# Performance work log

Hardware: AMD Instinct MI355X
Metric: run time of the kernel (lower is better)

The kernel has to match this reference:

```python
import jax, jax.numpy as jnp
import numpy as np

K = 3
STRIDE = 1
PAD = 1
DIL = 1


def _conv2d(x, w, b, stride, pad):
    y = jax.lax.conv_general_dilated(
        x, w, (stride, stride), [(pad, pad), (pad, pad)],
        dimension_numbers=('NCHW', 'OIHW', 'NCHW'))
    return y + b[None, :, None, None]


def setup_inputs() -> dict:
    key = jax.random.key(0)
    ks = jax.random.split(key, 6)
    N, Cin, Cout, H, W = 4, 64, 64, 128, 128
    x = jax.random.normal(ks[0], (N, Cin, H, W), jnp.float32)
    w_off = jax.random.normal(ks[1], (2 * K * K, Cin, K, K), jnp.float32) * 0.01
    b_off = jnp.zeros((2 * K * K,), jnp.float32)
    w_mask = jax.random.normal(ks[2], (K * K, Cin, K, K), jnp.float32) * 0.01
    b_mask = jnp.zeros((K * K,), jnp.float32)
    weight = jax.random.normal(ks[3], (Cout, Cin, K, K), jnp.float32) * 0.05
    bias = jax.random.normal(ks[4], (Cout,), jnp.float32)
    return {"x": x, "w_off": w_off, "b_off": b_off,
            "w_mask": w_mask, "b_mask": b_mask,
            "weight": weight, "bias": bias}


def _deform_conv(x, offset, weight, bias):
    # x: [N,C,H,W]; offset: [N,2*K2,Ho,Wo] with channel layout (dy,dx) per kernel pt
    N, C, H, W = x.shape
    K2 = K * K
    Ho, Wo = offset.shape[2], offset.shape[3]
    off_y = offset[:, 0::2]  # [N,K2,Ho,Wo]
    off_x = offset[:, 1::2]
    ki = jnp.arange(K2) // K
    kj = jnp.arange(K2) % K
    base_y = (jnp.arange(Ho) * STRIDE - PAD)[None, :, None] + (ki * DIL)[:, None, None]
    base_x = (jnp.arange(Wo) * STRIDE - PAD)[None, None, :] + (kj * DIL)[:, None, None]
    py = base_y[None].astype(off_y.dtype) + off_y  # [N,K2,Ho,Wo]
    px = base_x[None].astype(off_x.dtype) + off_x
    y0 = jnp.floor(py)
    x0 = jnp.floor(px)
    wy = py - y0
    wx = px - x0
    xf = x.reshape(N, C, H * W)

    def corner(yi, xi):
        valid = (yi >= 0) & (yi <= H - 1) & (xi >= 0) & (xi <= W - 1)
        yc = jnp.clip(yi, 0, H - 1).astype(jnp.int32)
        xc = jnp.clip(xi, 0, W - 1).astype(jnp.int32)
        idx = (yc * W + xc).reshape(N, -1)  # [N, K2*Ho*Wo]
        g = jnp.take_along_axis(xf, idx[:, None, :], axis=2)  # [N,C,K2*Ho*Wo]
        g = g.reshape(N, C, K2, Ho, Wo)
        return g * valid[:, None].astype(x.dtype)

    # bilinear interpolation with zero padding outside the image
    val = ((1 - wy) * (1 - wx))[:, None] * corner(y0, x0) \
        + ((1 - wy) * wx)[:, None] * corner(y0, x0 + 1) \
        + (wy * (1 - wx))[:, None] * corner(y0 + 1, x0) \
        + (wy * wx)[:, None] * corner(y0 + 1, x0 + 1)  # [N,C,K2,Ho,Wo]
    out = jnp.einsum('nckhw,ock->nohw', val,
                     weight.reshape(weight.shape[0], C, K2))
    return out + bias[None, :, None, None]


def reference(x, w_off, b_off, w_mask, b_mask, weight, bias):
    offset = _conv2d(x, w_off, b_off, STRIDE, PAD)              # [N,2*K2,Ho,Wo]
    mask = jax.nn.sigmoid(_conv2d(x, w_mask, b_mask, STRIDE, PAD))  # [N,K2,Ho,Wo]
    # source does mask.repeat(1,2,1,1) then offset*mask, then plain deform_conv2d
    offset = offset * jnp.concatenate([mask, mask], axis=1)
    return _deform_conv(x, offset, weight, bias)
```

## Files before the change

### kernel.cpp

```cpp
#include <hip/hip_runtime.h>
#include <math.h>

#define HD 128
#define WD 128
#define WP 130
#define CIN 64
#define COUT 64
#define NB 4
#define K2 9
#define HW (HD*WD)
#define CK 576
#define TP 16
#define NKK 18

#define WAM   (4 * NKK * 64 * 8)
#define WAO   (2 * NKK * 64 * 8)
#define XTP   ((size_t)NB * WP * WP * CIN)
#define OFFSZ ((size_t)NB * K2 * HW)
#define WTSZ  ((size_t)CK * COUT)

#define PRE_T 1024
#define PRE_H 65
#define PRE_P ((WAM + WAO) / 256)
#define HALO_PER_N 33024
#define HALO_W8 16512

typedef __attribute__((ext_vector_type(8))) short short8;
typedef __attribute__((ext_vector_type(4))) float f32x4;

__device__ inline unsigned short f2bf(float v) {
    unsigned int u = __float_as_uint(v);
    unsigned int r = u + 0x7fffu + ((u >> 16) & 1u);
    return (unsigned short)(r >> 16);
}
__device__ inline float bf2f(unsigned short b) {
    return __uint_as_float(((unsigned int)b) << 16);
}
__device__ inline unsigned int pack_bf16(float a, float b) {
#if __has_builtin(__builtin_amdgcn_cvt_pk_bf16_f32)
    auto r = __builtin_amdgcn_cvt_pk_bf16_f32(a, b);
    unsigned int u; __builtin_memcpy(&u, &r, 4); return u;
#else
    return ((unsigned int)f2bf(b) << 16) | (unsigned int)f2bf(a);
#endif
}

__global__ __launch_bounds__(256) void pre_kernel(
    const float* __restrict__ x,
    const float* __restrict__ weight,
    const float* __restrict__ w_off,
    const float* __restrict__ w_mask,
    unsigned short* __restrict__ xp,
    short* __restrict__ mhi, short* __restrict__ mlo,
    short* __restrict__ ohi, short* __restrict__ olo)
{
    __shared__ float tile[64][66];
    int bid = blockIdx.x;
    int t = threadIdx.x;

    if (bid < PRE_T) {
        int half = bid & 1;
        int h = (bid >> 1) & 127;
        int n = bid >> 8;
        int w0 = half * 64;
        int g = t >> 6, wl = t & 63;
        const float* xb = x + ((size_t)n * CIN) * HW + h * WD + w0;
        #pragma unroll
        for (int i = 0; i < 16; i++) {
            int cc = i * 4 + g;
            tile[wl][cc] = xb[(size_t)cc * HW + wl];
        }
        __syncthreads();
        size_t rowbase = (((size_t)n * WP + (h + 1)) * WP + (w0 + 1)) * CIN;
        #pragma unroll
        for (int i = 0; i < 8; i++) {
            int u = i * 256 + t;
            int ww = u >> 5;
            int cp = (u & 31) * 2;
            float2 v = *(const float2*)&tile[ww][cp];
            *(unsigned int*)&xp[rowbase + (size_t)ww * CIN + cp] = pack_bf16(v.x, v.y);
        }
    } else if (bid < PRE_T + PRE_H) {
        int widx = (bid - PRE_T) * 256 + t;
        if (widx < HALO_W8) {
            int s = widx * 8;
            int n = s / HALO_PER_N;
            int v = s - n * HALO_PER_N;
            size_t nb = (size_t)n * WP * WP * CIN;
            size_t base;
            if (v < 8320) {
                base = nb + v;
            } else if (v < 16640) {
                base = nb + (size_t)129 * WP * CIN + (v - 8320);
            } else if (v < 24832) {
                int v2 = v - 16640; int h = 1 + (v2 >> 6); int c = v2 & 63;
                base = nb + (size_t)h * WP * CIN + c;
            } else {
                int v3 = v - 24832; int h = 1 + (v3 >> 6); int c = v3 & 63;
                base = nb + ((size_t)h * WP + 129) * CIN + c;
            }
            short8 z = {0, 0, 0, 0, 0, 0, 0, 0};
            *(short8*)&xp[base] = z;
        }
    } else {
        int gid = (bid - PRE_T - PRE_H) * 256 + t;
        if (gid < WAM) {
            int idx = gid;
            int jj = idx & 7;
            int lane = (idx >> 3) & 63;
            int kk = (idx >> 9) % NKK;
            int mt = (idx >> 9) / NKK;
            int o = mt * 16 + (lane & 15);
            int rp = kk * 32 + (lane >> 4) * 8 + jj;
            int k = rp >> 6, c = rp & 63;
            float w = weight[((size_t)o * CIN + c) * 9 + k];
            unsigned short h = f2bf(w);
            mhi[idx] = (short)h;
            mlo[idx] = (short)f2bf(w - bf2f(h));
        } else {
            int idx = gid - WAM;
            int jj = idx & 7;
            int lane = (idx >> 3) & 63;
            int kk = (idx >> 9) % NKK;
            int mt = (idx >> 9) / NKK;
            int j = mt * 16 + (lane & 15);
            int rp = kk * 32 + (lane >> 4) * 8 + jj;
            int k = rp >> 6, c = rp & 63;
            float w = 0.f;
            if (j < 18)      w = w_off[((size_t)j * CIN + c) * 9 + k];
            else if (j < 27) w = w_mask[((size_t)(j - 18) * CIN + c) * 9 + k];
            unsigned short h = f2bf(w);
            ohi[idx] = (short)h;
            olo[idx] = (short)f2bf(w - bf2f(h));
        }
    }
}

__global__ __launch_bounds__(256) void fused_kernel(
    const unsigned short* __restrict__ xp,
    const short* __restrict__ waM_hi, const short* __restrict__ waM_lo,
    const short* __restrict__ waO_hi, const short* __restrict__ waO_lo,
    const float* __restrict__ b_off, const float* __restrict__ b_mask,
    const float* __restrict__ bias,
    float* __restrict__ out)
{
    __shared__ __align__(16) short val_hi[72 * 128];
    __shared__ float conv_s[27 * 17];
    __shared__ float4 p_w4[K2 * TP];
    __shared__ int4   p_idx4[K2 * TP];

    int t = threadIdx.x;
    int wv = t >> 6;
    int lane = t & 63;
    int wo0 = blockIdx.x * TP;
    int ho  = blockIdx.y;
    int n   = blockIdx.z;
    const unsigned short* xpn = xp + (size_t)n * WP * WP * CIN;
    int p16 = lane & 15, quad = lane >> 4;

    #pragma unroll
    for (int i = 0; i < 5; i++) {
        int u = t + 256 * i;
        if (u < K2 * TP * 8) {
            int tap = u >> 7;
            int p = (u >> 3) & 15;
            int g = u & 7;
            int ti = tap / 3, tj = tap - ti * 3;
            const short8 v = *(const short8*)&xpn[((size_t)(ho + ti) * WP + (wo0 + p + tj)) * CIN + g * 8];
            int c2 = tap * 8 + g;
            *(short8*)&val_hi[c2 * 128 + ((p + c2) & 15) * 8] = v;
        }
    }
    __syncthreads();

    if (wv < 2) {
        f32x4 acc = {0.f, 0.f, 0.f, 0.f};
        for (int kk = 0; kk < NKK; kk++) {
            int abase = ((wv * NKK + kk) * 64 + lane) * 8;
            short8 ah = *(const short8*)&waO_hi[abase];
            short8 al = *(const short8*)&waO_lo[abase];
            int c2 = kk * 4 + quad;
            short8 b = *(const short8*)&val_hi[c2 * 128 + ((p16 + c2) & 15) * 8];
            acc = __builtin_amdgcn_mfma_f32_16x16x32_bf16(ah, b, acc, 0, 0, 0);
            acc = __builtin_amdgcn_mfma_f32_16x16x32_bf16(al, b, acc, 0, 0, 0);
        }
        #pragma unroll
        for (int i = 0; i < 4; i++) {
            int j = wv * 16 + quad * 4 + i;
            if (j < 27) {
                float bv = (j < 18) ? b_off[j] : b_mask[j - 18];
                conv_s[j * 17 + p16] = acc[i] + bv;
            }
        }
    }
    __syncthreads();

    if (t < K2 * TP) {
        int k = t >> 4, p = t & 15;
        float oy_raw = conv_s[(2 * k) * 17 + p];
        float ox_raw = conv_s[(2 * k + 1) * 17 + p];
        float my = 1.f / (1.f + expf(-conv_s[(18 + (2 * k) % 9) * 17 + p]));
        float mx = 1.f / (1.f + expf(-conv_s[(18 + (2 * k + 1) % 9) * 17 + p]));
        float oy = oy_raw * my;
        float ox = ox_raw * mx;
        int ki = k / 3, kj = k - ki * 3;
        int wo = wo0 + p;
        float py = (float)(ho - 1 + ki) + oy;
        float px = (float)(wo - 1 + kj) + ox;
        float y0f = floorf(py), x0f = floorf(px);
        float wy = py - y0f, wx = px - x0f;
        int y0 = (int)y0f, x0 = (int)x0f;
        float wy0 = 1.f - wy, wx0 = 1.f - wx;
        int y0c = min(max(y0, 0), HD - 1);
        int y1c = min(max(y0 + 1, 0), HD - 1);
        int x0c = min(max(x0, 0), WD - 1);
        int x1c = min(max(x0 + 1, 0), WD - 1);
        bool vy0 = (y0 >= 0) && (y0 < HD);
        bool vy1 = (y0 + 1 >= 0) && (y0 + 1 < HD);
        bool vx0 = (x0 >= 0) && (x0 < WD);
        bool vx1 = (x0 + 1 >= 0) && (x0 + 1 < WD);
        float4 w4;
        w4.x = (vy0 && vx0) ? wy0 * wx0 : 0.f;
        w4.y = (vy0 && vx1) ? wy0 * wx  : 0.f;
        w4.z = (vy1 && vx0) ? wy  * wx0 : 0.f;
        w4.w = (vy1 && vx1) ? wy  * wx  : 0.f;
        int4 i4;
        i4.x = ((y0c + 1) * WP + (x0c + 1)) * CIN;
        i4.y = ((y0c + 1) * WP + (x1c + 1)) * CIN;
        i4.z = ((y1c + 1) * WP + (x0c + 1)) * CIN;
        i4.w = ((y1c + 1) * WP + (x1c + 1)) * CIN;
        p_w4[t] = w4;
        p_idx4[t] = i4;
    }
    __syncthreads();

    {
        int sub = lane >> 4;
        int c0 = (lane & 15) * 4;
        #pragma unroll
        for (int i = 0; i < 9; i++) {
            int task = i * 16 + wv * 4 + sub;
            int k = task >> 4, p = task & 15;
            float4 w4 = p_w4[task];
            int4  i4 = p_idx4[task];
            uint2 qa = *(const uint2*)&xpn[i4.x + c0];
            uint2 qb = *(const uint2*)&xpn[i4.y + c0];
            uint2 qc = *(const uint2*)&xpn[i4.z + c0];
            uint2 qd = *(const uint2*)&xpn[i4.w + c0];
            float g0 = w4.x * __uint_as_float(qa.x << 16)
                     + w4.y * __uint_as_float(qb.x << 16)
                     + w4.z * __uint_as_float(qc.x << 16)
                     + w4.w * __uint_as_float(qd.x << 16);
            float g1 = w4.x * __uint_as_float(qa.x & 0xffff0000u)
                     + w4.y * __uint_as_float(qb.x & 0xffff0000u)
                     + w4.z * __uint_as_float(qc.x & 0xffff0000u)
                     + w4.w * __uint_as_float(qd.x & 0xffff0000u);
            float g2 = w4.x * __uint_as_float(qa.y << 16)
                     + w4.y * __uint_as_float(qb.y << 16)
                     + w4.z * __uint_as_float(qc.y << 16)
                     + w4.w * __uint_as_float(qd.y << 16);
            float g3 = w4.x * __uint_as_float(qa.y & 0xffff0000u)
                     + w4.y * __uint_as_float(qb.y & 0xffff0000u)
                     + w4.z * __uint_as_float(qc.y & 0xffff0000u)
                     + w4.w * __uint_as_float(qd.y & 0xffff0000u);
            uint2 r;
            r.x = pack_bf16(g0, g1);
            r.y = pack_bf16(g2, g3);
            int c2 = k * 8 + (c0 >> 3);
            int jj = c0 & 7;
            *(uint2*)&val_hi[c2 * 128 + ((p + c2) & 15) * 8 + jj] = r;
        }
    }
    __syncthreads();

    f32x4 acc = {0.f, 0.f, 0.f, 0.f};
    for (int kk = 0; kk < NKK; kk++) {
        int abase = ((wv * NKK + kk) * 64 + lane) * 8;
        short8 ah = *(const short8*)&waM_hi[abase];
        short8 al = *(const short8*)&waM_lo[abase];
        int c2 = kk * 4 + quad;
        short8 b = *(const short8*)&val_hi[c2 * 128 + ((p16 + c2) & 15) * 8];
        acc = __builtin_amdgcn_mfma_f32_16x16x32_bf16(ah, b, acc, 0, 0, 0);
        acc = __builtin_amdgcn_mfma_f32_16x16x32_bf16(al, b, acc, 0, 0, 0);
    }
    __syncthreads();
    float* os = (float*)val_hi;
    #pragma unroll
    for (int i = 0; i < 4; i++) {
        int o = wv * 16 + quad * 4 + i;
        os[o * 17 + p16] = acc[i] + bias[o];
    }
    __syncthreads();

    size_t obase = ((size_t)n * COUT) * HW + (size_t)ho * WD + wo0;
    #pragma unroll
    for (int i = 0; i < 4; i++) {
        int l = t + 256 * i;
        int oo = l >> 4, p = l & 15;
        out[obase + (size_t)oo * HW + p] = os[oo * 17 + p];
    }
}

__global__ void transpose_w_kernel(const float* __restrict__ w, float* __restrict__ wt) {
    int i = blockIdx.x * 256 + threadIdx.x;
    int o = i / CK;
    int ck = i - o * CK;
    wt[ck * COUT + o] = w[i];
}

__global__ __launch_bounds__(256) void offmask_kernel(
    const float* __restrict__ x,
    const float* __restrict__ w_off, const float* __restrict__ b_off,
    const float* __restrict__ w_mask, const float* __restrict__ b_mask,
    float* __restrict__ offy, float* __restrict__ offx)
{
    __shared__ float ws[CK][27];
    int t = threadIdx.x;
    for (int i = t; i < CK * 27; i += 256) {
        int j = i % 27;
        int citap = i / 27;
        int ci = citap / 9;
        int tap = citap - ci * 9;
        float v;
        if (j < 18) v = w_off[(j * CIN + ci) * 9 + tap];
        else        v = w_mask[((j - 18) * CIN + ci) * 9 + tap];
        ws[citap][j] = v;
    }
    __syncthreads();

    int pix = blockIdx.x * 256 + t;
    int n  = pix >> 14;
    int ho = (pix >> 7) & 127;
    int wo = pix & 127;

    float acc[27];
    #pragma unroll
    for (int j = 0; j < 18; j++) acc[j] = b_off[j];
    #pragma unroll
    for (int j = 0; j < 9; j++)  acc[18 + j] = b_mask[j];

    int offs[9];
    bool oks[9];
    #pragma unroll
    for (int dy = 0; dy < 3; dy++) {
        int y = ho - 1 + dy;
        #pragma unroll
        for (int dx = 0; dx < 3; dx++) {
            int xx = wo - 1 + dx;
            bool ok = (y >= 0) && (y < HD) && (xx >= 0) && (xx < WD);
            oks[dy * 3 + dx] = ok;
            offs[dy * 3 + dx] = (ok ? y : 0) * WD + (ok ? xx : 0);
        }
    }
    const float* xn = x + (size_t)n * CIN * HW;
    for (int ci = 0; ci < CIN; ci++) {
        const float* xc = xn + (size_t)ci * HW;
        float v[9];
        #pragma unroll
        for (int tap = 0; tap < 9; tap++)
            v[tap] = oks[tap] ? xc[offs[tap]] : 0.f;
        #pragma unroll
        for (int tap = 0; tap < 9; tap++) {
            const float* wrow = ws[ci * 9 + tap];
            float vv = v[tap];
            #pragma unroll
            for (int j = 0; j < 27; j++) acc[j] += wrow[j] * vv;
        }
    }
    float m[9];
    #pragma unroll
    for (int j = 0; j < 9; j++) m[j] = 1.f / (1.f + expf(-acc[18 + j]));
    #pragma unroll
    for (int k = 0; k < 9; k++) {
        int cy = 2 * k, cx = 2 * k + 1;
        float my = m[cy < 9 ? cy : cy - 9];
        float mx = m[cx < 9 ? cx : cx - 9];
        size_t o = (((size_t)n * K2 + k) * HD + ho) * WD + wo;
        offy[o] = acc[cy] * my;
        offx[o] = acc[cx] * mx;
    }
}

__global__ __launch_bounds__(256) void deform_kernel(
    const float* __restrict__ x,
    const float* __restrict__ offy, const float* __restrict__ offx,
    const float* __restrict__ wt,
    const float* __restrict__ bias,
    float* __restrict__ out)
{
    __shared__ __align__(16) float val_s[CK * TP];
    __shared__ float4 p_w4[K2 * TP];
    __shared__ int4   p_idx4[K2 * TP];

    int t = threadIdx.x;
    int wo0 = blockIdx.x * TP;
    int ho  = blockIdx.y;
    int n   = blockIdx.z;

    if (t < K2 * TP) {
        int k = t >> 4, p = t & 15;
        int wo = wo0 + p;
        size_t oi = (((size_t)n * K2 + k) * HD + ho) * WD + wo;
        float oy = offy[oi], ox = offx[oi];
        int ki = k / 3, kj = k - ki * 3;
        float py = (float)(ho - 1 + ki) + oy;
        float px = (float)(wo - 1 + kj) + ox;
        float y0f = floorf(py), x0f = floorf(px);
        float wy = py - y0f, wx = px - x0f;
        int y0 = (int)y0f, x0 = (int)x0f;
        float wy0 = 1.f - wy, wx0 = 1.f - wx;
        int y0c = min(max(y0, 0), HD - 1);
        int y1c = min(max(y0 + 1, 0), HD - 1);
        int x0c = min(max(x0, 0), WD - 1);
        int x1c = min(max(x0 + 1, 0), WD - 1);
        bool vy0 = (y0 >= 0) && (y0 < HD);
        bool vy1 = (y0 + 1 >= 0) && (y0 + 1 < HD);
        bool vx0 = (x0 >= 0) && (x0 < WD);
        bool vx1 = (x0 + 1 >= 0) && (x0 + 1 < WD);
        float4 w4;
        w4.x = (vy0 && vx0) ? wy0 * wx0 : 0.f;
        w4.y = (vy0 && vx1) ? wy0 * wx  : 0.f;
        w4.z = (vy1 && vx0) ? wy  * wx0 : 0.f;
        w4.w = (vy1 && vx1) ? wy  * wx  : 0.f;
        int4 i4;
        i4.x = y0c * WD + x0c;
        i4.y = y0c * WD + x1c;
        i4.z = y1c * WD + x0c;
        i4.w = y1c * WD + x1c;
        p_w4[t] = w4;
        p_idx4[t] = i4;
    }
    __syncthreads();

    const float* xn = x + (size_t)n * CIN * HW;
    for (int e = t; e < CK * TP; e += 256) {
        int row = e >> 4, p = e & 15;
        int cc = row / 9, k = row - cc * 9;
        int task = (k << 4) | p;
        float4 w4 = p_w4[task];
        int4  i4 = p_idx4[task];
        const float* xc = xn + (size_t)cc * HW;
        val_s[e] = w4.x * xc[i4.x] + w4.y * xc[i4.y]
                 + w4.z * xc[i4.z] + w4.w * xc[i4.w];
    }
    __syncthreads();

    int o = t & 63, q = t >> 6;
    float4 acc = {0.f, 0.f, 0.f, 0.f};
    const float4* v4 = (const float4*)val_s;
    const float* wp = wt + o;
    #pragma unroll 4
    for (int r = 0; r < CK; r++) {
        float w = wp[r * COUT];
        float4 vv = v4[r * 4 + q];
        acc.x += w * vv.x; acc.y += w * vv.y;
        acc.z += w * vv.z; acc.w += w * vv.w;
    }
    float b = bias[o];
    acc.x += b; acc.y += b; acc.z += b; acc.w += b;
    __syncthreads();
    float4* o4 = (float4*)val_s;
    o4[o * 4 + q] = acc;
    __syncthreads();
    size_t obase = ((size_t)n * COUT) * HW + (size_t)ho * WD + wo0;
    #pragma unroll
    for (int i = 0; i < 4; i++) {
        int l = t + 256 * i;
        int oo = l >> 4, p = l & 15;
        out[obase + (size_t)oo * HW + p] = val_s[l];
    }
}

extern "C" void kernel_launch(void* const* d_in, const int* in_sizes, int n_in,
                              void* d_out, int out_size, void* d_ws, size_t ws_size,
                              hipStream_t stream) {
    const float* x      = (const float*)d_in[0];
    const float* w_off  = (const float*)d_in[1];
    const float* b_off  = (const float*)d_in[2];
    const float* w_mask = (const float*)d_in[3];
    const float* b_mask = (const float*)d_in[4];
    const float* weight = (const float*)d_in[5];
    const float* bias   = (const float*)d_in[6];
    float* out = (float*)d_out;

    short* base = (short*)d_ws;
    short* waM_hi = base;
    short* waM_lo = waM_hi + WAM;
    short* waO_hi = waM_lo + WAM;
    short* waO_lo = waO_hi + WAO;
    unsigned short* xp = (unsigned short*)(waO_lo + WAO);
    size_t need = ((size_t)2 * WAM + 2 * WAO + XTP) * sizeof(short);

    if (ws_size >= need) {
        pre_kernel<<<PRE_T + PRE_H + PRE_P, 256, 0, stream>>>(
            x, weight, w_off, w_mask, xp, waM_hi, waM_lo, waO_hi, waO_lo);
        fused_kernel<<<dim3(WD / TP, HD, NB), 256, 0, stream>>>(
            xp, waM_hi, waM_lo, waO_hi, waO_lo, b_off, b_mask, bias, out);
    } else {
        float* offy = (float*)d_ws;
        float* offx = offy + OFFSZ;
        float* wt   = offx + OFFSZ;
        transpose_w_kernel<<<144, 256, 0, stream>>>(weight, wt);
        offmask_kernel<<<256, 256, 0, stream>>>(x, w_off, b_off, w_mask, b_mask, offy, offx);
        deform_kernel<<<dim3(WD / TP, HD, NB), 256, 0, stream>>>(x, offy, offx, wt, bias, out);
    }
}
```

Measured before the change: 134.8 us.

## Split offset conv across all waves, dual accumulators, packed indices, direct output stores

The offset/mask MFMA conv now runs on all four waves, with the K dimension split in half and two partial sums combined in shared memory. The hi and lo MFMA chains use separate accumulators to break the serial dependency. Gather indices are packed into one 32-bit word instead of an int4, and the kernel gets an occupancy hint of 6 blocks. The final output skips the LDS staging and its two syncs and is stored straight from registers, which risks less coalesced 16-float store segments.

After: 128.7 us. 1.05x faster.

```diff
diff --git a/kernel.cpp b/kernel.cpp
--- a/kernel.cpp
+++ b/kernel.cpp
@@ -136,7 +136,7 @@
     }
 }
 
-__global__ __launch_bounds__(256) void fused_kernel(
+__global__ __launch_bounds__(256, 6) void fused_kernel(
     const unsigned short* __restrict__ xp,
     const short* __restrict__ waM_hi, const short* __restrict__ waM_lo,
     const short* __restrict__ waO_hi, const short* __restrict__ waO_lo,
@@ -145,9 +145,9 @@
     float* __restrict__ out)
 {
     __shared__ __align__(16) short val_hi[72 * 128];
-    __shared__ float conv_s[27 * 17];
+    __shared__ float conv_h[2][27 * 17];
     __shared__ float4 p_w4[K2 * TP];
-    __shared__ int4   p_idx4[K2 * TP];
+    __shared__ unsigned int p_pk[K2 * TP];
 
     int t = threadIdx.x;
     int wv = t >> 6;
@@ -173,34 +173,41 @@
     }
     __syncthreads();
 
-    if (wv < 2) {
-        f32x4 acc = {0.f, 0.f, 0.f, 0.f};
-        for (int kk = 0; kk < NKK; kk++) {
-            int abase = ((wv * NKK + kk) * 64 + lane) * 8;
+    {
+        int jt = wv & 1, kh = wv >> 1;
+        f32x4 acc_h = {0.f, 0.f, 0.f, 0.f};
+        f32x4 acc_l = {0.f, 0.f, 0.f, 0.f};
+        #pragma unroll
+        for (int q = 0; q < 9; q++) {
+            int kk = kh * 9 + q;
+            int abase = ((jt * NKK + kk) * 64 + lane) * 8;
             short8 ah = *(const short8*)&waO_hi[abase];
             short8 al = *(const short8*)&waO_lo[abase];
             int c2 = kk * 4 + quad;
             short8 b = *(const short8*)&val_hi[c2 * 128 + ((p16 + c2) & 15) * 8];
-            acc = __builtin_amdgcn_mfma_f32_16x16x32_bf16(ah, b, acc, 0, 0, 0);
-            acc = __builtin_amdgcn_mfma_f32_16x16x32_bf16(al, b, acc, 0, 0, 0);
+            acc_h = __builtin_amdgcn_mfma_f32_16x16x32_bf16(ah, b, acc_h, 0, 0, 0);
+            acc_l = __builtin_amdgcn_mfma_f32_16x16x32_bf16(al, b, acc_l, 0, 0, 0);
         }
         #pragma unroll
         for (int i = 0; i < 4; i++) {
-            int j = wv * 16 + quad * 4 + i;
-            if (j < 27) {
-                float bv = (j < 18) ? b_off[j] : b_mask[j - 18];
-                conv_s[j * 17 + p16] = acc[i] + bv;
-            }
+            int j = jt * 16 + quad * 4 + i;
+            if (j < 27) conv_h[kh][j * 17 + p16] = acc_h[i] + acc_l[i];
         }
     }
     __syncthreads();
 
     if (t < K2 * TP) {
         int k = t >> 4, p = t & 15;
-        float oy_raw = conv_s[(2 * k) * 17 + p];
-        float ox_raw = conv_s[(2 * k + 1) * 17 + p];
-        float my = 1.f / (1.f + expf(-conv_s[(18 + (2 * k) % 9) * 17 + p]));
-        float mx = 1.f / (1.f + expf(-conv_s[(18 + (2 * k + 1) % 9) * 17 + p]));
+        int r0 = (2 * k) * 17 + p;
+        int r1 = (2 * k + 1) * 17 + p;
+        int rm0 = (18 + (2 * k) % 9) * 17 + p;
+        int rm1 = (18 + (2 * k + 1) % 9) * 17 + p;
+        float oy_raw = conv_h[0][r0] + conv_h[1][r0] + b_off[2 * k];
+        float ox_raw = conv_h[0][r1] + conv_h[1][r1] + b_off[2 * k + 1];
+        float sm0 = conv_h[0][rm0] + conv_h[1][rm0] + b_mask[(2 * k) % 9];
+        float sm1 = conv_h[0][rm1] + conv_h[1][rm1] + b_mask[(2 * k + 1) % 9];
+        float my = 1.f / (1.f + expf(-sm0));
+        float mx = 1.f / (1.f + expf(-sm1));
         float oy = oy_raw * my;
         float ox = ox_raw * mx;
         int ki = k / 3, kj = k - ki * 3;
@@ -224,13 +231,9 @@
         w4.y = (vy0 && vx1) ? wy0 * wx  : 0.f;
         w4.z = (vy1 && vx0) ? wy  * wx0 : 0.f;
         w4.w = (vy1 && vx1) ? wy  * wx  : 0.f;
-        int4 i4;
-        i4.x = ((y0c + 1) * WP + (x0c + 1)) * CIN;
-        i4.y = ((y0c + 1) * WP + (x1c + 1)) * CIN;
-        i4.z = ((y1c + 1) * WP + (x0c + 1)) * CIN;
-        i4.w = ((y1c + 1) * WP + (x1c + 1)) * CIN;
         p_w4[t] = w4;
-        p_idx4[t] = i4;
+        p_pk[t] = (unsigned int)(y0c + 1) | ((unsigned int)(y1c + 1) << 8)
+                | ((unsigned int)(x0c + 1) << 16) | ((unsigned int)(x1c + 1) << 24);
     }
     __syncthreads();
 
@@ -242,11 +245,15 @@
             int task = i * 16 + wv * 4 + sub;
             int k = task >> 4, p = task & 15;
             float4 w4 = p_w4[task];
-            int4  i4 = p_idx4[task];
-            uint2 qa = *(const uint2*)&xpn[i4.x + c0];
-            uint2 qb = *(const uint2*)&xpn[i4.y + c0];
-            uint2 qc = *(const uint2*)&xpn[i4.z + c0];
-            uint2 qd = *(const uint2*)&xpn[i4.w + c0];
+            unsigned int pk = p_pk[task];
+            int y0b = (int)(pk & 255) * (WP * CIN);
+            int y1b = (int)((pk >> 8) & 255) * (WP * CIN);
+            int x0b = (int)((pk >> 16) & 255) * CIN + c0;
+            int x1b = (int)(pk >> 24) * CIN + c0;
+            uint2 qa = *(const uint2*)&xpn[y0b + x0b];
+            uint2 qb = *(const uint2*)&xpn[y0b + x1b];
+            uint2 qc = *(const uint2*)&xpn[y1b + x0b];
+            uint2 qd = *(const uint2*)&xpn[y1b + x1b];
             float g0 = w4.x * __uint_as_float(qa.x << 16)
                      + w4.y * __uint_as_float(qb.x << 16)
                      + w4.z * __uint_as_float(qc.x << 16)
@@ -273,31 +280,24 @@
     }
     __syncthreads();
 
-    f32x4 acc = {0.f, 0.f, 0.f, 0.f};
+    f32x4 acc_h = {0.f, 0.f, 0.f, 0.f};
+    f32x4 acc_l = {0.f, 0.f, 0.f, 0.f};
+    #pragma unroll
     for (int kk = 0; kk < NKK; kk++) {
         int abase = ((wv * NKK + kk) * 64 + lane) * 8;
         short8 ah = *(const short8*)&waM_hi[abase];
         short8 al = *(const short8*)&waM_lo[abase];
         int c2 = kk * 4 + quad;
         short8 b = *(const short8*)&val_hi[c2 * 128 + ((p16 + c2) & 15) * 8];
-        acc = __builtin_amdgcn_mfma_f32_16x16x32_bf16(ah, b, acc, 0, 0, 0);
-        acc = __builtin_amdgcn_mfma_f32_16x16x32_bf16(al, b, acc, 0, 0, 0);
-    }
-    __syncthreads();
-    float* os = (float*)val_hi;
+        acc_h = __builtin_amdgcn_mfma_f32_16x16x32_bf16(ah, b, acc_h, 0, 0, 0);
+        acc_l = __builtin_amdgcn_mfma_f32_16x16x32_bf16(al, b, acc_l, 0, 0, 0);
+    }
+
+    size_t obase = ((size_t)n * COUT) * HW + (size_t)ho * WD + wo0;
     #pragma unroll
     for (int i = 0; i < 4; i++) {
         int o = wv * 16 + quad * 4 + i;
-        os[o * 17 + p16] = acc[i] + bias[o];
-    }
-    __syncthreads();
-
-    size_t obase = ((size_t)n * COUT) * HW + (size_t)ho * WD + wo0;
-    #pragma unroll
-    for (int i = 0; i < 4; i++) {
-        int l = t + 256 * i;
-        int oo = l >> 4, p = l & 15;
-        out[obase + (size_t)oo * HW + p] = os[oo * 17 + p];
+        out[obase + (size_t)o * HW + p16] = acc_h[i] + acc_l[i] + bias[o];
     }
 }
 
```

## Widen fused deformable-conv tile to 32 pixels and reuse weight fragments

Applied to the files above, without the earlier changes.

Doubles the output pixels per block in the fused kernel from 16 to 32. Each wave now computes two 16-pixel MFMA tiles that share the same hi/lo weight fragments, and all four waves take part in the offset/mask conv instead of two. Results are written straight from the accumulators to global memory, dropping the LDS staging pass and one barrier. In exchange the LDS footprint and register pressure grow, a launch-bounds occupancy hint is added, and the grid has half as many blocks.

Result: faster. 124.8 us (-7.4%).

```diff
diff --git a/kernel.cpp b/kernel.cpp
--- a/kernel.cpp
+++ b/kernel.cpp
@@ -10,7 +10,8 @@
 #define K2 9
 #define HW (HD*WD)
 #define CK 576
-#define TP 16
+#define TP 32
+#define TPF 16
 #define NKK 18
 
 #define WAM   (4 * NKK * 64 * 8)
@@ -43,6 +44,12 @@
 #else
     return ((unsigned int)f2bf(b) << 16) | (unsigned int)f2bf(a);
 #endif
+}
+__device__ inline float2 up2(unsigned int u) {
+    float2 r;
+    r.x = __uint_as_float(u << 16);
+    r.y = __uint_as_float(u & 0xffff0000u);
+    return r;
 }
 
 __global__ __launch_bounds__(256) void pre_kernel(
@@ -136,7 +143,7 @@
     }
 }
 
-__global__ __launch_bounds__(256) void fused_kernel(
+__global__ __launch_bounds__(256, 3) void fused_kernel(
     const unsigned short* __restrict__ xp,
     const short* __restrict__ waM_hi, const short* __restrict__ waM_lo,
     const short* __restrict__ waO_hi, const short* __restrict__ waO_lo,
@@ -144,8 +151,8 @@
     const float* __restrict__ bias,
     float* __restrict__ out)
 {
-    __shared__ __align__(16) short val_hi[72 * 128];
-    __shared__ float conv_s[27 * 17];
+    __shared__ __align__(16) short val_hi[72 * 256];
+    __shared__ float conv_s[27 * 32];
     __shared__ float4 p_w4[K2 * TP];
     __shared__ int4   p_idx4[K2 * TP];
 
@@ -159,145 +166,138 @@
     int p16 = lane & 15, quad = lane >> 4;
 
     #pragma unroll
-    for (int i = 0; i < 5; i++) {
+    for (int i = 0; i < 9; i++) {
         int u = t + 256 * i;
-        if (u < K2 * TP * 8) {
-            int tap = u >> 7;
-            int p = (u >> 3) & 15;
-            int g = u & 7;
-            int ti = tap / 3, tj = tap - ti * 3;
-            const short8 v = *(const short8*)&xpn[((size_t)(ho + ti) * WP + (wo0 + p + tj)) * CIN + g * 8];
-            int c2 = tap * 8 + g;
-            *(short8*)&val_hi[c2 * 128 + ((p + c2) & 15) * 8] = v;
-        }
-    }
-    __syncthreads();
-
-    if (wv < 2) {
-        f32x4 acc = {0.f, 0.f, 0.f, 0.f};
+        int tap = u >> 8;
+        int p = (u >> 3) & 31;
+        int g = u & 7;
+        int ti = tap / 3, tj = tap - ti * 3;
+        const short8 v = *(const short8*)&xpn[((size_t)(ho + ti) * WP + (wo0 + p + tj)) * CIN + g * 8];
+        int c2 = tap * 8 + g;
+        *(short8*)&val_hi[c2 * 256 + ((p + c2) & 31) * 8] = v;
+    }
+    __syncthreads();
+
+    {
+        int jt = wv >> 1, pt = wv & 1;
+        f32x4 acc_h = {0.f, 0.f, 0.f, 0.f};
+        f32x4 acc_l = {0.f, 0.f, 0.f, 0.f};
+        #pragma unroll
         for (int kk = 0; kk < NKK; kk++) {
-            int abase = ((wv * NKK + kk) * 64 + lane) * 8;
+            int abase = ((jt * NKK + kk) * 64 + lane) * 8;
             short8 ah = *(const short8*)&waO_hi[abase];
             short8 al = *(const short8*)&waO_lo[abase];
             int c2 = kk * 4 + quad;
-            short8 b = *(const short8*)&val_hi[c2 * 128 + ((p16 + c2) & 15) * 8];
-            acc = __builtin_amdgcn_mfma_f32_16x16x32_bf16(ah, b, acc, 0, 0, 0);
-            acc = __builtin_amdgcn_mfma_f32_16x16x32_bf16(al, b, acc, 0, 0, 0);
+            short8 b = *(const short8*)&val_hi[c2 * 256 + ((pt * 16 + p16 + c2) & 31) * 8];
+            acc_h = __builtin_amdgcn_mfma_f32_16x16x32_bf16(ah, b, acc_h, 0, 0, 0);
+            acc_l = __builtin_amdgcn_mfma_f32_16x16x32_bf16(al, b, acc_l, 0, 0, 0);
         }
         #pragma unroll
         for (int i = 0; i < 4; i++) {
-            int j = wv * 16 + quad * 4 + i;
+            int j = jt * 16 + quad * 4 + i;
             if (j < 27) {
                 float bv = (j < 18) ? b_off[j] : b_mask[j - 18];
-                conv_s[j * 17 + p16] = acc[i] + bv;
+                conv_s[j * 32 + pt * 16 + p16] = acc_h[i] + acc_l[i] + bv;
             }
         }
     }
     __syncthreads();
 
-    if (t < K2 * TP) {
-        int k = t >> 4, p = t & 15;
-        float oy_raw = conv_s[(2 * k) * 17 + p];
-        float ox_raw = conv_s[(2 * k + 1) * 17 + p];
-        float my = 1.f / (1.f + expf(-conv_s[(18 + (2 * k) % 9) * 17 + p]));
-        float mx = 1.f / (1.f + expf(-conv_s[(18 + (2 * k + 1) % 9) * 17 + p]));
-        float oy = oy_raw * my;
-        float ox = ox_raw * mx;
-        int ki = k / 3, kj = k - ki * 3;
-        int wo = wo0 + p;
-        float py = (float)(ho - 1 + ki) + oy;
-        float px = (float)(wo - 1 + kj) + ox;
-        float y0f = floorf(py), x0f = floorf(px);
-        float wy = py - y0f, wx = px - x0f;
-        int y0 = (int)y0f, x0 = (int)x0f;
-        float wy0 = 1.f - wy, wx0 = 1.f - wx;
-        int y0c = min(max(y0, 0), HD - 1);
-        int y1c = min(max(y0 + 1, 0), HD - 1);
-        int x0c = min(max(x0, 0), WD - 1);
-        int x1c = min(max(x0 + 1, 0), WD - 1);
-        bool vy0 = (y0 >= 0) && (y0 < HD);
-        bool vy1 = (y0 + 1 >= 0) && (y0 + 1 < HD);
-        bool vx0 = (x0 >= 0) && (x0 < WD);
-        bool vx1 = (x0 + 1 >= 0) && (x0 + 1 < WD);
-        float4 w4;
-        w4.x = (vy0 && vx0) ? wy0 * wx0 : 0.f;
-        w4.y = (vy0 && vx1) ? wy0 * wx  : 0.f;
-        w4.z = (vy1 && vx0) ? wy  * wx0 : 0.f;
-        w4.w = (vy1 && vx1) ? wy  * wx  : 0.f;
-        int4 i4;
-        i4.x = ((y0c + 1) * WP + (x0c + 1)) * CIN;
-        i4.y = ((y0c + 1) * WP + (x1c + 1)) * CIN;
-        i4.z = ((y1c + 1) * WP + (x0c + 1)) * CIN;
-        i4.w = ((y1c + 1) * WP + (x1c + 1)) * CIN;
-        p_w4[t] = w4;
-        p_idx4[t] = i4;
-    }
-    __syncthreads();
-
-    {
-        int sub = lane >> 4;
-        int c0 = (lane & 15) * 4;
-        #pragma unroll
-        for (int i = 0; i < 9; i++) {
-            int task = i * 16 + wv * 4 + sub;
-            int k = task >> 4, p = task & 15;
-            float4 w4 = p_w4[task];
-            int4  i4 = p_idx4[task];
-            uint2 qa = *(const uint2*)&xpn[i4.x + c0];
-            uint2 qb = *(const uint2*)&xpn[i4.y + c0];
-            uint2 qc = *(const uint2*)&xpn[i4.z + c0];
-            uint2 qd = *(const uint2*)&xpn[i4.w + c0];
-            float g0 = w4.x * __uint_as_float(qa.x << 16)
-                     + w4.y * __uint_as_float(qb.x << 16)
-                     + w4.z * __uint_as_float(qc.x << 16)
-                     + w4.w * __uint_as_float(qd.x << 16);
-            float g1 = w4.x * __uint_as_float(qa.x & 0xffff0000u)
-                     + w4.y * __uint_as_float(qb.x & 0xffff0000u)
-                     + w4.z * __uint_as_float(qc.x & 0xffff0000u)
-                     + w4.w * __uint_as_float(qd.x & 0xffff0000u);
-            float g2 = w4.x * __uint_as_float(qa.y << 16)
-                     + w4.y * __uint_as_float(qb.y << 16)
-                     + w4.z * __uint_as_float(qc.y << 16)
-                     + w4.w * __uint_as_float(qd.y << 16);
-            float g3 = w4.x * __uint_as_float(qa.y & 0xffff0000u)
-                     + w4.y * __uint_as_float(qb.y & 0xffff0000u)
-                     + w4.z * __uint_as_float(qc.y & 0xffff0000u)
-                     + w4.w * __uint_as_float(qd.y & 0xffff0000u);
-            uint2 r;
-            r.x = pack_bf16(g0, g1);
-            r.y = pack_bf16(g2, g3);
-            int c2 = k * 8 + (c0 >> 3);
-            int jj = c0 & 7;
-            *(uint2*)&val_hi[c2 * 128 + ((p + c2) & 15) * 8 + jj] = r;
-        }
-    }
-    __syncthreads();
-
-    f32x4 acc = {0.f, 0.f, 0.f, 0.f};
+    #pragma unroll
+    for (int pass = 0; pass < 2; pass++) {
+        int u = t + pass * 256;
+        if (u < K2 * TP) {
+            int k = u >> 5, p = u & 31;
+            float oy_raw = conv_s[(2 * k) * 32 + p];
+            float ox_raw = conv_s[(2 * k + 1) * 32 + p];
+            float my = 1.f / (1.f + expf(-conv_s[(18 + (2 * k) % 9) * 32 + p]));
+            float mx = 1.f / (1.f + expf(-conv_s[(18 + (2 * k + 1) % 9) * 32 + p]));
+            float oy = oy_raw * my;
+            float ox = ox_raw * mx;
+            int ki = k / 3, kj = k - ki * 3;
+            int wo = wo0 + p;
+            float py = (float)(ho - 1 + ki) + oy;
+            float px = (float)(wo - 1 + kj) + ox;
+            float y0f = floorf(py), x0f = floorf(px);
+            float wy = py - y0f, wx = px - x0f;
+            int y0 = (int)y0f, x0 = (int)x0f;
+            float wy0 = 1.f - wy, wx0 = 1.f - wx;
+            int y0c = min(max(y0, 0), HD - 1);
+            int y1c = min(max(y0 + 1, 0), HD - 1);
+            int x0c = min(max(x0, 0), WD - 1);
+            int x1c = min(max(x0 + 1, 0), WD - 1);
+            bool vy0 = (y0 >= 0) && (y0 < HD);
+            bool vy1 = (y0 + 1 >= 0) && (y0 + 1 < HD);
+            bool vx0 = (x0 >= 0) && (x0 < WD);
+            bool vx1 = (x0 + 1 >= 0) && (x0 + 1 < WD);
+            float4 w4;
+            w4.x = (vy0 && vx0) ? wy0 * wx0 : 0.f;
+            w4.y = (vy0 && vx1) ? wy0 * wx  : 0.f;
+            w4.z = (vy1 && vx0) ? wy  * wx0 : 0.f;
+            w4.w = (vy1 && vx1) ? wy  * wx  : 0.f;
+            int4 i4;
+            i4.x = ((y0c + 1) * WP + (x0c + 1)) * CIN;
+            i4.y = ((y0c + 1) * WP + (x1c + 1)) * CIN;
+            i4.z = ((y1c + 1) * WP + (x0c + 1)) * CIN;
+            i4.w = ((y1c + 1) * WP + (x1c + 1)) * CIN;
+            p_w4[u] = w4;
+            p_idx4[u] = i4;
+        }
+    }
+    __syncthreads();
+
+    #pragma unroll
+    for (int i = 0; i < 18; i++) {
+        int u = t + 256 * i;
+        int task = u >> 4;
+        int c0 = (u & 15) * 4;
+        int k = task >> 5, p = task & 31;
+        float4 w4 = p_w4[task];
+        int4  i4 = p_idx4[task];
+        uint2 qa = *(const uint2*)&xpn[i4.x + c0];
+        uint2 qb = *(const uint2*)&xpn[i4.y + c0];
+        uint2 qc = *(const uint2*)&xpn[i4.z + c0];
+        uint2 qd = *(const uint2*)&xpn[i4.w + c0];
+        float2 ga = up2(qa.x), gb = up2(qb.x), gc = up2(qc.x), gd = up2(qd.x);
+        float2 g01;
+        g01.x = w4.x * ga.x + w4.y * gb.x + w4.z * gc.x + w4.w * gd.x;
+        g01.y = w4.x * ga.y + w4.y * gb.y + w4.z * gc.y + w4.w * gd.y;
+        float2 ha = up2(qa.y), hb = up2(qb.y), hc = up2(qc.y), hd = up2(qd.y);
+        float2 g23;
+        g23.x = w4.x * ha.x + w4.y * hb.x + w4.z * hc.x + w4.w * hd.x;
+        g23.y = w4.x * ha.y + w4.y * hb.y + w4.z * hc.y + w4.w * hd.y;
+        uint2 r;
+        r.x = pack_bf16(g01.x, g01.y);
+        r.y = pack_bf16(g23.x, g23.y);
+        int c2 = k * 8 + (c0 >> 3);
+        int jj = c0 & 7;
+        *(uint2*)&val_hi[c2 * 256 + ((p + c2) & 31) * 8 + jj] = r;
+    }
+    __syncthreads();
+
+    f32x4 a0 = {0.f, 0.f, 0.f, 0.f};
+    f32x4 a1 = {0.f, 0.f, 0.f, 0.f};
+    #pragma unroll
     for (int kk = 0; kk < NKK; kk++) {
         int abase = ((wv * NKK + kk) * 64 + lane) * 8;
         short8 ah = *(const short8*)&waM_hi[abase];
         short8 al = *(const short8*)&waM_lo[abase];
         int c2 = kk * 4 + quad;
-        short8 b = *(const short8*)&val_hi[c2 * 128 + ((p16 + c2) & 15) * 8];
-        acc = __builtin_amdgcn_mfma_f32_16x16x32_bf16(ah, b, acc, 0, 0, 0);
-        acc = __builtin_amdgcn_mfma_f32_16x16x32_bf16(al, b, acc, 0, 0, 0);
-    }
-    __syncthreads();
-    float* os = (float*)val_hi;
+        short8 b0 = *(const short8*)&val_hi[c2 * 256 + ((p16 + c2) & 31) * 8];
+        short8 b1 = *(const short8*)&val_hi[c2 * 256 + ((16 + p16 + c2) & 31) * 8];
+        a0 = __builtin_amdgcn_mfma_f32_16x16x32_bf16(ah, b0, a0, 0, 0, 0);
+        a1 = __builtin_amdgcn_mfma_f32_16x16x32_bf16(ah, b1, a1, 0, 0, 0);
+        a0 = __builtin_amdgcn_mfma_f32_16x16x32_bf16(al, b0, a0, 0, 0, 0);
+        a1 = __builtin_amdgcn_mfma_f32_16x16x32_bf16(al, b1, a1, 0, 0, 0);
+    }
+
+    size_t obase = ((size_t)n * COUT) * HW + (size_t)ho * WD + wo0;
     #pragma unroll
     for (int i = 0; i < 4; i++) {
         int o = wv * 16 + quad * 4 + i;
-        os[o * 17 + p16] = acc[i] + bias[o];
-    }
-    __syncthreads();
-
-    size_t obase = ((size_t)n * COUT) * HW + (size_t)ho * WD + wo0;
-    #pragma unroll
-    for (int i = 0; i < 4; i++) {
-        int l = t + 256 * i;
-        int oo = l >> 4, p = l & 15;
-        out[obase + (size_t)oo * HW + p] = os[oo * 17 + p];
+        float bv = bias[o];
+        out[obase + (size_t)o * HW + p16] = a0[i] + bv;
+        out[obase + (size_t)o * HW + 16 + p16] = a1[i] + bv;
     }
 }
 
@@ -388,16 +388,16 @@
     const float* __restrict__ bias,
     float* __restrict__ out)
 {
-    __shared__ __align__(16) float val_s[CK * TP];
-    __shared__ float4 p_w4[K2 * TP];
-    __shared__ int4   p_idx4[K2 * TP];
+    __shared__ __align__(16) float val_s[CK * TPF];
+    __shared__ float4 p_w4[K2 * TPF];
+    __shared__ int4   p_idx4[K2 * TPF];
 
     int t = threadIdx.x;
-    int wo0 = blockIdx.x * TP;
+    int wo0 = blockIdx.x * TPF;
     int ho  = blockIdx.y;
     int n   = blockIdx.z;
 
-    if (t < K2 * TP) {
+    if (t < K2 * TPF) {
         int k = t >> 4, p = t & 15;
         int wo = wo0 + p;
         size_t oi = (((size_t)n * K2 + k) * HD + ho) * WD + wo;
@@ -433,7 +433,7 @@
     __syncthreads();
 
     const float* xn = x + (size_t)n * CIN * HW;
-    for (int e = t; e < CK * TP; e += 256) {
+    for (int e = t; e < CK * TPF; e += 256) {
         int row = e >> 4, p = e & 15;
         int cc = row / 9, k = row - cc * 9;
         int task = (k << 4) | p;
@@ -502,6 +502,6 @@
         float* wt   = offx + OFFSZ;
         transpose_w_kernel<<<144, 256, 0, stream>>>(weight, wt);
         offmask_kernel<<<256, 256, 0, stream>>>(x, w_off, b_off, w_mask, b_mask, offy, offx);
-        deform_kernel<<<dim3(WD / TP, HD, NB), 256, 0, stream>>>(x, offy, offx, wt, bias, out);
-    }
-}
+        deform_kernel<<<dim3(WD / TPF, HD, NB), 256, 0, stream>>>(x, offy, offx, wt, bias, out);
+    }
+}
```
